# Performance work log

Hardware: AMD Instinct MI355X
Metric: run time of the kernel (lower is better)

Reference implementation:

```python
import jax, jax.numpy as jnp
import numpy as np

NUM_TOKENS = 1048576
NUM_EXPERTS = 64


def setup_inputs() -> dict:
    key = jax.random.key(0)
    router_logits_fp32 = jax.random.normal(key, (NUM_TOKENS, NUM_EXPERTS), dtype=jnp.float32)
    return {"router_logits_fp32": router_logits_fp32, "top_k": 8}


def reference(router_logits_fp32, top_k):
    # Fused softmax over experts + top-k selection (aiter.topk_softmax with renorm=True).
    probs = jax.nn.softmax(router_logits_fp32, axis=-1)          # [T, E]
    topk_weights, topk_ids = jax.lax.top_k(probs, top_k)         # [T, K], [T, K]
    # renormalize selected weights to sum to 1 per token (the trailing True flag)
    topk_weights = topk_weights / jnp.sum(topk_weights, axis=-1, keepdims=True)
    num_tokens = router_logits_fp32.shape[0]
    # token_expert_indices[t, k] = t * top_k + k (row-major source-row mapping used
    # later for the token permutation/scatter into expert buffers)
    token_expert_indices = jnp.arange(num_tokens * top_k, dtype=jnp.int32).reshape(num_tokens, top_k)
    return topk_weights, topk_ids.astype(jnp.int32), token_expert_indices
```

## Files before the change

kernel.cpp:

```cpp
#include <hip/hip_runtime.h>
#include <stdint.h>


typedef float f32x4 __attribute__((ext_vector_type(4)));

#define DPP_QUAD_XOR1   0xB1
#define DPP_QUAD_XOR2   0x4E
#define DPP_HALF_MIRROR 0x141

template<int CTRL>
static __device__ __forceinline__ double dpp64d(double x) {
    uint64_t b = (uint64_t)__double_as_longlong(x);
    int lo = __builtin_amdgcn_update_dpp(0, (int)(uint32_t)b,         CTRL, 0xF, 0xF, true);
    int hi = __builtin_amdgcn_update_dpp(0, (int)(uint32_t)(b >> 32), CTRL, 0xF, 0xF, true);
    uint64_t r = ((uint64_t)(uint32_t)hi << 32) | (uint32_t)lo;
    return __longlong_as_double((long long)r);
}

template<int CTRL>
static __device__ __forceinline__ float dppf(float x) {
    int i = __builtin_amdgcn_update_dpp(0, __float_as_int(x), CTRL, 0xF, 0xF, true);
    return __int_as_float(i);
}

#define CED(x, y) { double hi_ = fmax(x, y), lo_ = fmin(x, y); x = hi_; y = lo_; }

template<int CTRL>
static __device__ __forceinline__ void merge_level(double k[8]) {
    double m[8];
#pragma unroll
    for (int i = 0; i < 8; ++i) {
        double p = dpp64d<CTRL>(k[7 - i]);
        m[i] = fmax(k[i], p);
    }
    CED(m[0], m[4]) CED(m[1], m[5]) CED(m[2], m[6]) CED(m[3], m[7])
    CED(m[0], m[2]) CED(m[1], m[3]) CED(m[4], m[6]) CED(m[5], m[7])
    CED(m[0], m[1]) CED(m[2], m[3]) CED(m[4], m[5]) CED(m[6], m[7])
#pragma unroll
    for (int i = 0; i < 8; ++i) k[i] = m[i];
}

__global__ __launch_bounds__(256) void topk_softmax_k(
    const float* __restrict__ logits,
    float* __restrict__ out_w,
    float* __restrict__ out_id,
    float* __restrict__ out_tei,
    int T)
{
    const int  lane = threadIdx.x & 63;
    const int  wv   = (int)(threadIdx.x >> 6);
    const long t0   = (long)blockIdx.x * 32 + (long)wv * 8;
    if (t0 >= T) return;

    const int  sub = lane & 7;
    const bool act = (t0 + (lane >> 3)) < T;

    const f32x4* src = reinterpret_cast<const f32x4*>(logits)
                     + (act ? (t0 * 16 + (long)lane * 2) : 0);
    f32x4 a = __builtin_nontemporal_load(src);
    f32x4 b = __builtin_nontemporal_load(src + 1);

    const float vals[8] = {a.x, a.y, a.z, a.w, b.x, b.y, b.z, b.w};
    const double base = (double)(63 - sub * 8) * 0.015625;

    double k[8];
#pragma unroll
    for (int j = 0; j < 8; ++j) {
        uint32_t u = __float_as_uint(vals[j]);
        uint32_t o = (u & 0x80000000u) ? ~u : (u | 0x80000000u);
        k[j] = (double)o + (base - j * 0.015625);
    }

    CED(k[0],k[1]) CED(k[2],k[3]) CED(k[4],k[5]) CED(k[6],k[7])
    CED(k[0],k[2]) CED(k[1],k[3]) CED(k[4],k[6]) CED(k[5],k[7])
    CED(k[1],k[2]) CED(k[5],k[6])
    CED(k[0],k[4]) CED(k[1],k[5]) CED(k[2],k[6]) CED(k[3],k[7])
    CED(k[2],k[4]) CED(k[3],k[5])
    CED(k[1],k[2]) CED(k[3],k[4]) CED(k[5],k[6])

    merge_level<DPP_QUAD_XOR1>(k);
    merge_level<DPP_QUAD_XOR2>(k);
    merge_level<DPP_HALF_MIRROR>(k);

    double t4a = (sub & 4) ? k[4] : k[0];
    double t4b = (sub & 4) ? k[5] : k[1];
    double t4c = (sub & 4) ? k[6] : k[2];
    double t4d = (sub & 4) ? k[7] : k[3];
    double t2a = (sub & 2) ? t4c : t4a;
    double t2b = (sub & 2) ? t4d : t4b;
    double sel = (sub & 1) ? t2b : t2a;

    uint32_t o0 = (uint32_t)k[0];
    uint32_t mb = (o0 & 0x80000000u) ? (o0 & 0x7fffffffu) : ~o0;
    float    mv = __uint_as_float(mb);

    uint32_t os   = (uint32_t)sel;
    double   frac = sel - (double)os;
    int      cidx = (int)(frac * 64.0 + 0.5);
    int      idx  = 63 - cidx;
    uint32_t ub   = (os & 0x80000000u) ? (os & 0x7fffffffu) : ~os;
    float    v    = __uint_as_float(ub);

    float e = __expf(v - mv);
    float s = e;
    s += dppf<DPP_QUAD_XOR1>(s);
    s += dppf<DPP_QUAD_XOR2>(s);
    s += dppf<DPP_HALF_MIRROR>(s);
    float wgt = e * __builtin_amdgcn_rcpf(s);

    if (act) {
        const long oi = t0 * 8 + lane;
        __builtin_nontemporal_store(wgt,        &out_w[oi]);
        __builtin_nontemporal_store((float)idx, &out_id[oi]);
        __builtin_nontemporal_store((float)oi,  &out_tei[oi]);
    }
}

extern "C" void kernel_launch(void* const* d_in, const int* in_sizes, int n_in,
                              void* d_out, int out_size, void* d_ws, size_t ws_size,
                              hipStream_t stream) {
    const float* logits = (const float*)d_in[0];
    const int T = in_sizes[0] / 64;

    float* outw = (float*)d_out;
    float* outi = outw + (size_t)T * 8;
    float* outt = outi + (size_t)T * 8;

    const int blocks = (T + 31) / 32;
    hipLaunchKernelGGL(topk_softmax_k, dim3(blocks), dim3(256), 0, stream,
                       logits, outw, outi, outt, T);
}
```

Before: 78.12 us.

## Convert to persistent grid-stride kernel with software-prefetched next group loads

Replaces the one-group-per-wave launch of 32768 blocks with a fixed grid of up to 2048 blocks whose waves loop over 8-token groups in grid-stride order. Each iteration loads the next group's logits before processing the current one, so memory latency overlaps with the sort and softmax work. This cuts block launch overhead and keeps loads in flight, at the cost of fewer resident waves when the grid is small and an extra redundant load on the last iteration. The tail of a partial final group no longer clamps its load addresses, so a partial last group could read past the input buffer.

After: 80.56 us. +3.1%, slower.

```diff
diff --git a/kernel.cpp b/kernel.cpp
--- a/kernel.cpp
+++ b/kernel.cpp
@@ -47,72 +47,83 @@
     float* __restrict__ out_tei,
     int T)
 {
-    const int  lane = threadIdx.x & 63;
-    const int  wv   = (int)(threadIdx.x >> 6);
-    const long t0   = (long)blockIdx.x * 32 + (long)wv * 8;
-    if (t0 >= T) return;
+    const int lane = threadIdx.x & 63;
+    const int wv   = (int)(threadIdx.x >> 6);
+    const int sub  = lane & 7;
 
-    const int  sub = lane & 7;
-    const bool act = (t0 + (lane >> 3)) < T;
+    const long ng = ((long)T + 7) >> 3;
+    const long gs = (long)gridDim.x * 4;
+    long g = (long)blockIdx.x * 4 + wv;
+    if (g >= ng) return;
 
-    const f32x4* src = reinterpret_cast<const f32x4*>(logits)
-                     + (act ? (t0 * 16 + (long)lane * 2) : 0);
-    f32x4 a = __builtin_nontemporal_load(src);
-    f32x4 b = __builtin_nontemporal_load(src + 1);
+    const f32x4* __restrict__ base = reinterpret_cast<const f32x4*>(logits);
+    const double kbase = (double)(63 - sub * 8) * 0.015625;
 
-    const float vals[8] = {a.x, a.y, a.z, a.w, b.x, b.y, b.z, b.w};
-    const double base = (double)(63 - sub * 8) * 0.015625;
+    f32x4 a0 = __builtin_nontemporal_load(base + g * 128 + lane * 2);
+    f32x4 b0 = __builtin_nontemporal_load(base + g * 128 + lane * 2 + 1);
 
-    double k[8];
+    while (g < ng) {
+        const long gn  = g + gs;
+        const long gnc = (gn < ng) ? gn : g;
+        f32x4 a1 = __builtin_nontemporal_load(base + gnc * 128 + lane * 2);
+        f32x4 b1 = __builtin_nontemporal_load(base + gnc * 128 + lane * 2 + 1);
+
+        const float vals[8] = {a0.x, a0.y, a0.z, a0.w, b0.x, b0.y, b0.z, b0.w};
+        double k[8];
 #pragma unroll
-    for (int j = 0; j < 8; ++j) {
-        uint32_t u = __float_as_uint(vals[j]);
-        uint32_t o = (u & 0x80000000u) ? ~u : (u | 0x80000000u);
-        k[j] = (double)o + (base - j * 0.015625);
-    }
+        for (int j = 0; j < 8; ++j) {
+            uint32_t u = __float_as_uint(vals[j]);
+            uint32_t o = (u & 0x80000000u) ? ~u : (u | 0x80000000u);
+            k[j] = (double)o + (kbase - j * 0.015625);
+        }
 
-    CED(k[0],k[1]) CED(k[2],k[3]) CED(k[4],k[5]) CED(k[6],k[7])
-    CED(k[0],k[2]) CED(k[1],k[3]) CED(k[4],k[6]) CED(k[5],k[7])
-    CED(k[1],k[2]) CED(k[5],k[6])
-    CED(k[0],k[4]) CED(k[1],k[5]) CED(k[2],k[6]) CED(k[3],k[7])
-    CED(k[2],k[4]) CED(k[3],k[5])
-    CED(k[1],k[2]) CED(k[3],k[4]) CED(k[5],k[6])
+        CED(k[0],k[1]) CED(k[2],k[3]) CED(k[4],k[5]) CED(k[6],k[7])
+        CED(k[0],k[2]) CED(k[1],k[3]) CED(k[4],k[6]) CED(k[5],k[7])
+        CED(k[1],k[2]) CED(k[5],k[6])
+        CED(k[0],k[4]) CED(k[1],k[5]) CED(k[2],k[6]) CED(k[3],k[7])
+        CED(k[2],k[4]) CED(k[3],k[5])
+        CED(k[1],k[2]) CED(k[3],k[4]) CED(k[5],k[6])
 
-    merge_level<DPP_QUAD_XOR1>(k);
-    merge_level<DPP_QUAD_XOR2>(k);
-    merge_level<DPP_HALF_MIRROR>(k);
+        merge_level<DPP_QUAD_XOR1>(k);
+        merge_level<DPP_QUAD_XOR2>(k);
+        merge_level<DPP_HALF_MIRROR>(k);
 
-    double t4a = (sub & 4) ? k[4] : k[0];
-    double t4b = (sub & 4) ? k[5] : k[1];
-    double t4c = (sub & 4) ? k[6] : k[2];
-    double t4d = (sub & 4) ? k[7] : k[3];
-    double t2a = (sub & 2) ? t4c : t4a;
-    double t2b = (sub & 2) ? t4d : t4b;
-    double sel = (sub & 1) ? t2b : t2a;
+        double t4a = (sub & 4) ? k[4] : k[0];
+        double t4b = (sub & 4) ? k[5] : k[1];
+        double t4c = (sub & 4) ? k[6] : k[2];
+        double t4d = (sub & 4) ? k[7] : k[3];
+        double t2a = (sub & 2) ? t4c : t4a;
+        double t2b = (sub & 2) ? t4d : t4b;
+        double sel = (sub & 1) ? t2b : t2a;
 
-    uint32_t o0 = (uint32_t)k[0];
-    uint32_t mb = (o0 & 0x80000000u) ? (o0 & 0x7fffffffu) : ~o0;
-    float    mv = __uint_as_float(mb);
+        uint32_t o0 = (uint32_t)k[0];
+        uint32_t mb = (o0 & 0x80000000u) ? (o0 & 0x7fffffffu) : ~o0;
+        float    mv = __uint_as_float(mb);
 
-    uint32_t os   = (uint32_t)sel;
-    double   frac = sel - (double)os;
-    int      cidx = (int)(frac * 64.0 + 0.5);
-    int      idx  = 63 - cidx;
-    uint32_t ub   = (os & 0x80000000u) ? (os & 0x7fffffffu) : ~os;
-    float    v    = __uint_as_float(ub);
+        uint32_t os   = (uint32_t)sel;
+        double   frac = sel - (double)os;
+        int      cidx = (int)(frac * 64.0 + 0.5);
+        int      idx  = 63 - cidx;
+        uint32_t ub   = (os & 0x80000000u) ? (os & 0x7fffffffu) : ~os;
+        float    v    = __uint_as_float(ub);
 
-    float e = __expf(v - mv);
-    float s = e;
-    s += dppf<DPP_QUAD_XOR1>(s);
-    s += dppf<DPP_QUAD_XOR2>(s);
-    s += dppf<DPP_HALF_MIRROR>(s);
-    float wgt = e * __builtin_amdgcn_rcpf(s);
+        float e = __expf(v - mv);
+        float s = e;
+        s += dppf<DPP_QUAD_XOR1>(s);
+        s += dppf<DPP_QUAD_XOR2>(s);
+        s += dppf<DPP_HALF_MIRROR>(s);
+        float wgt = e * __builtin_amdgcn_rcpf(s);
 
-    if (act) {
-        const long oi = t0 * 8 + lane;
-        __builtin_nontemporal_store(wgt,        &out_w[oi]);
-        __builtin_nontemporal_store((float)idx, &out_id[oi]);
-        __builtin_nontemporal_store((float)oi,  &out_tei[oi]);
+        const long t0 = g * 8;
+        if (t0 + (lane >> 3) < T) {
+            const long oi = t0 * 8 + lane;
+            __builtin_nontemporal_store(wgt,        &out_w[oi]);
+            __builtin_nontemporal_store((float)idx, &out_id[oi]);
+            __builtin_nontemporal_store((float)oi,  &out_tei[oi]);
+        }
+
+        a0 = a1; b0 = b1;
+        g = gn;
     }
 }
 
@@ -126,7 +137,9 @@
     float* outi = outw + (size_t)T * 8;
     float* outt = outi + (size_t)T * 8;
 
-    const int blocks = (T + 31) / 32;
-    hipLaunchKernelGGL(topk_softmax_k, dim3(blocks), dim3(256), 0, stream,
+    const long ng = ((long)T + 7) >> 3;
+    long blocks = 2048;
+    if (blocks > (ng + 3) / 4) blocks = (ng + 3) / 4;
+    hipLaunchKernelGGL(topk_softmax_k, dim3((uint32_t)blocks), dim3(256), 0, stream,
                        logits, outw, outi, outt, T);
 }
```
